# Kernel tuning notes

Measured on AMD Instinct MI355X. Metric: run time of the kernel, lower is better.

## Reference

```python
import math
import jax, jax.numpy as jnp
import numpy as np

B, S, E, H, P = 8, 1024, 512, 8, 32
MAXD, OFFS, LW, STL, HID = 256, 8.0, 4, 4, 2048

def _lin(x, w, b):
    return x @ w.T + b

def _gelu(x):
    return jax.nn.gelu(x, approximate=False)  # torch nn.GELU default (erf)

def _ln(x, g, b, eps=1e-5):
    m = x.mean(-1, keepdims=True)
    v = ((x - m) ** 2).mean(-1, keepdims=True)
    return (x - m) / jnp.sqrt(v + eps) * g + b

def setup_inputs() -> dict:
    key = jax.random.key(0)
    ks = iter(jax.random.split(key, 40))
    def w(*shape):
        return (jax.random.normal(next(ks), shape, dtype=jnp.float32) * 0.02)
    x = jax.random.normal(next(ks), (B, S, E), dtype=jnp.float32)
    lengths = jax.random.randint(next(ks), (B,), S // 2, S + 1)
    padding_mask = jnp.arange(S)[None, :] >= lengths[:, None]  # (B,S) bool
    inp = dict(x=x, padding_mask=padding_mask)
    # local MHA (torch nn.MultiheadAttention packed in_proj)
    inp.update(in_proj_w=w(3 * E, E), in_proj_b=jnp.zeros((3 * E,), jnp.float32),
               mha_out_w=w(E, E), mha_out_b=jnp.zeros((E,), jnp.float32))
    # deformable attention projections
    for nm in ('dq', 'dk', 'dv', 'do'):
        inp[nm + '_w'] = w(E, E); inp[nm + '_b'] = jnp.zeros((E,), jnp.float32)
    inp.update(off1_w=w(E, E), off1_b=jnp.zeros((E,), jnp.float32),
               off2_w=w(H * P, E), off2_b=jnp.zeros((H * P,), jnp.float32))
    inp.update(gate1_w=w(E, 3 * E), gate1_b=jnp.zeros((E,), jnp.float32),
               gate2_w=w(E, E), gate2_b=jnp.zeros((E,), jnp.float32))
    inp.update(n1_g=jnp.ones((E,), jnp.float32), n1_b=jnp.zeros((E,), jnp.float32),
               n2_g=jnp.ones((E,), jnp.float32), n2_b=jnp.zeros((E,), jnp.float32))
    inp.update(ffn1_w=w(HID, E), ffn1_b=jnp.zeros((HID,), jnp.float32),
               ffn2_w=w(E, HID), ffn2_b=jnp.zeros((E,), jnp.float32))
    return inp

def _forward(x, padding_mask, in_proj_w, in_proj_b, mha_out_w, mha_out_b,
             dq_w, dq_b, dk_w, dk_b, dv_w, dv_b, do_w, do_b,
             off1_w, off1_b, off2_w, off2_b, gate1_w, gate1_b, gate2_w, gate2_b,
             n1_g, n1_b, n2_g, n2_b, ffn1_w, ffn1_b, ffn2_w, ffn2_b):
    Bv, Sv, Ev = x.shape
    hd = Ev // H
    pos = jnp.arange(Sv)
    # ---------------- local causal windowed MHA ----------------
    qkv = _lin(x, in_proj_w, in_proj_b)
    q, k, v = jnp.split(qkv, 3, axis=-1)
    q = q.reshape(Bv, Sv, H, hd).transpose(0, 2, 1, 3)  # bhsd
    k = k.reshape(Bv, Sv, H, hd).transpose(0, 2, 1, 3)
    v = v.reshape(Bv, Sv, H, hd).transpose(0, 2, 1, 3)
    scores = jnp.einsum('bhqd,bhkd->bhqk', q, k) / math.sqrt(hd)
    future = pos[None, :] > pos[:, None]
    too_far = (pos[:, None] - pos[None, :]) >= min(LW, STL)
    lmask = (future | too_far)[None, None] | padding_mask[:, None, None, :]
    scores = jnp.where(lmask, -jnp.inf, scores)
    allm = lmask.all(-1, keepdims=True)
    scores = jnp.where(allm, 0.0, scores)  # avoid NaN on fully-masked (padded) rows
    attn = jax.nn.softmax(scores, axis=-1)
    attn = jnp.where(lmask, 0.0, attn)
    lo = jnp.einsum('bhqk,bhkd->bhqd', attn, v).transpose(0, 2, 1, 3).reshape(Bv, Sv, Ev)
    local_out = _lin(lo, mha_out_w, mha_out_b)
    # ---------------- deformable long-history attention ----------------
    anchors = jnp.linspace(0.1, 0.9, P)
    valid_len = jnp.clip(Sv - padding_mask.sum(-1), 1, None)
    positions = pos[None, :, None].astype(jnp.float32)  # (1,S,1)
    base = anchors[None, None, :] * positions
    off = jnp.tanh(_lin(_gelu(_lin(x, off1_w, off1_b)), off2_w, off2_b))
    off = off.reshape(Bv, Sv, H, P).mean(2) * OFFS
    sampled = base + off
    sampled = jnp.clip(sampled, jnp.clip(positions - MAXD, 0, None), positions)
    sampled = jnp.minimum(sampled, (valid_len - 1).astype(jnp.float32)[:, None, None])
    sp = jnp.round(sampled).astype(jnp.int32)  # (B,S,P) sample positions
    qd = _lin(x, dq_w, dq_b)
    kd = _lin(x, dk_w, dk_b)
    vd = _lin(x, dv_w, dv_b)
    bidx = jnp.arange(Bv)[:, None, None]
    k_sp = kd[bidx, sp]  # (B,S,P,E) gathered keys
    v_sp = vd[bidx, sp]
    sc = jnp.einsum('bqd,bqpd->bqp', qd, k_sp) / math.sqrt(Ev)
    samp_inv = padding_mask[bidx, sp]
    causal_inv = sp > pos[None, :, None]
    rb = jnp.clip(pos[:, None] - (STL - 1), 0, None)
    long_mem_mask = pos[None, :] >= rb  # (S,S): forbid recent short-term positions
    extra_inv = long_mem_mask[pos[None, :, None], sp]
    inv = samp_inv | causal_inv | extra_inv
    sc = jnp.where(inv, -jnp.inf, sc)
    alli = inv.all(-1, keepdims=True)
    sc = jnp.where(alli, 0.0, sc)
    a = jax.nn.softmax(sc, axis=-1)
    a = jnp.where(inv, 0.0, a)
    long_out = _lin(jnp.einsum('bqp,bqpd->bqd', a, v_sp), do_w, do_b)
    # ---------------- gate fuse + FFN ----------------
    cat = jnp.concatenate([x, local_out, long_out], axis=-1)
    g = jax.nn.sigmoid(_lin(_gelu(_lin(cat, gate1_w, gate1_b)), gate2_w, gate2_b))
    fused = g * local_out + (1.0 - g) * long_out
    x1 = _ln(x + fused, n1_g, n1_b)
    f = _lin(_gelu(_lin(x1, ffn1_w, ffn1_b)), ffn2_w, ffn2_b)
    return _ln(x1 + f, n2_g, n2_b)

def reference(x, padding_mask, in_proj_w, in_proj_b, mha_out_w, mha_out_b,
              dq_w, dq_b, dk_w, dk_b, dv_w, dv_b, do_w, do_b,
              off1_w, off1_b, off2_w, off2_b, gate1_w, gate1_b, gate2_w, gate2_b,
              n1_g, n1_b, n2_g, n2_b, ffn1_w, ffn1_b, ffn2_w, ffn2_b):
    return _forward(x, padding_mask, in_proj_w, in_proj_b, mha_out_w, mha_out_b,
                    dq_w, dq_b, dk_w, dk_b, dv_w, dv_b, do_w, do_b,
                    off1_w, off1_b, off2_w, off2_b, gate1_w, gate1_b, gate2_w, gate2_b,
                    n1_g, n1_b, n2_g, n2_b, ffn1_w, ffn1_b, ffn2_w, ffn2_b)
```

## Files before the change

kernel.cpp:

```cpp
#include <hip/hip_runtime.h>
#include <hip/hip_bf16.h>
#include <type_traits>

typedef __hip_bfloat16 bf16;
typedef __attribute__((ext_vector_type(8))) short short8;
typedef __attribute__((ext_vector_type(4))) float floatx4;

static constexpr int kB = 8;
static constexpr int kS = 1024;
static constexpr int kE = 512;
static constexpr int kH = 8;
static constexpr int kP = 32;
static constexpr int kTok = kB * kS;
static constexpr int kHid = 2048;

__device__ __forceinline__ void load8f(const bf16* p, float* f) {
  uint4 u = *(const uint4*)p;
  const bf16* h = (const bf16*)&u;
#pragma unroll
  for (int e = 0; e < 8; e++) f[e] = __bfloat162float(h[e]);
}
__device__ __forceinline__ void store8b(bf16* p, const float* f) {
  uint4 u;
  bf16* h = (bf16*)&u;
#pragma unroll
  for (int e = 0; e < 8; e++) h[e] = __float2bfloat16(f[e]);
  *(uint4*)p = u;
}
__device__ __forceinline__ bool is_pad(const void* pm, int flag, int idx) {
  return flag ? (((const int*)pm)[idx] != 0)
              : (((const unsigned char*)pm)[idx] != 0);
}

__global__ __launch_bounds__(256) void detect_kernel(const void* __restrict__ x,
                                                     int* __restrict__ meta) {
  __shared__ int cnt;
  if (threadIdx.x == 0) cnt = 0;
  __syncthreads();
  const unsigned short* u = (const unsigned short*)x;
  int c = 0;
  for (int i = threadIdx.x; i < 1024; i += 256) {
    int e = (u[i] >> 7) & 0xFF;
    if (e >= 0x90) c++;
  }
  if (c) atomicAdd(&cnt, c);
  __syncthreads();
  if (threadIdx.x == 0) meta[9] = (cnt > 64) ? 1 : 0;
}

__global__ __launch_bounds__(256) void meta_kernel(const void* __restrict__ pm,
                                                   int* __restrict__ meta) {
  __shared__ int bigfound;
  __shared__ int cnt[kB];
  int tid = threadIdx.x;
  if (tid == 0) bigfound = 0;
  if (tid < kB) cnt[tid] = 0;
  __syncthreads();
  const unsigned int* w = (const unsigned int*)pm;
  int f = 0;
  for (int i = tid; i < 2048; i += 256)
    if (w[i] & 0xFFFFFFFEu) f = 1;
  if (f) atomicOr(&bigfound, 1);
  __syncthreads();
  int flag = bigfound ? 0 : 1;
  for (int i = tid; i < kTok; i += 256) {
    if (is_pad(pm, flag, i)) atomicAdd(&cnt[i >> 10], 1);
  }
  __syncthreads();
  if (tid == 0) meta[0] = flag;
  if (tid < kB) {
    int vl = kS - cnt[tid];
    if (vl < 1) vl = 1;
    meta[1 + tid] = vl;
  }
}

struct CvtJob { const void* src; bf16* hi; bf16* lo; int nblk; };
struct CvtJobs { CvtJob j[13]; };
__global__ __launch_bounds__(256) void cvt_all_kernel(CvtJobs jobs,
                                                      const int* __restrict__ meta) {
  int fp = meta[9];
  int b = blockIdx.x, ji = 0;
  while (b >= jobs.j[ji].nblk) { b -= jobs.j[ji].nblk; ji++; }
  CvtJob J = jobs.j[ji];
  int i = b * 1024 + threadIdx.x * 4;
  float v[4];
  if (fp) {
    float4 f = ((const float4*)J.src)[i >> 2];
    v[0] = f.x; v[1] = f.y; v[2] = f.z; v[3] = f.w;
  } else {
    uint2 u = *(const uint2*)((const bf16*)J.src + i);
    const bf16* h = (const bf16*)&u;
#pragma unroll
    for (int e = 0; e < 4; e++) v[e] = __bfloat162float(h[e]);
  }
  uint2 uh;
  bf16* hh = (bf16*)&uh;
#pragma unroll
  for (int e = 0; e < 4; e++) hh[e] = __float2bfloat16(v[e]);
  *(uint2*)(J.hi + i) = uh;
  if (J.lo) {
    uint2 ul;
    bf16* hl = (bf16*)&ul;
#pragma unroll
    for (int e = 0; e < 4; e++)
      hl[e] = __float2bfloat16(v[e] - __bfloat162float(hh[e]));
    *(uint2*)(J.lo + i) = ul;
  }
}

struct CvtFJob { const void* src; float* dst; int n; };
struct CvtFJobs { CvtFJob j[16]; };
__global__ __launch_bounds__(256) void cvt_small_kernel(CvtFJobs jobs,
                                                        const int* __restrict__ meta) {
  int fp = meta[9];
#pragma unroll 1
  for (int ji = 0; ji < 16; ji++) {
    CvtFJob J = jobs.j[ji];
    for (int i = threadIdx.x; i < J.n; i += 256)
      J.dst[i] = fp ? ((const float*)J.src)[i]
                    : __bfloat162float(((const bf16*)J.src)[i]);
  }
}

static constexpr int BK = 32, LDK = 40;

template <int BM, int BN, int ACT, bool ACC, typename OUTT>
__global__ __launch_bounds__(256) void gemm_bt(
    const bf16* __restrict__ A, const bf16* __restrict__ W,
    const float* __restrict__ bias, OUTT* __restrict__ C, int M, int N,
    int K) {
  constexpr int WR = (BM == 128 && BN == 128) ? 4 : 2;
  constexpr int WC = (BN == 128) ? 4 : 4;
  __shared__ bf16 As[BM * LDK];
  __shared__ bf16 Bs[BN * LDK];
  const int tid = threadIdx.x;
  const int lane = tid & 63;
  const int wid = tid >> 6;
  int wm, wn;
  if constexpr (BM == 128 && BN == 128) {
    wm = (wid >> 1) * 64; wn = (wid & 1) * 64;
  } else {
    wm = wid * 32; wn = 0;
  }
  const int m0 = blockIdx.x * BM, n0 = blockIdx.y * BN;

  floatx4 acc[WR][WC];
#pragma unroll
  for (int i = 0; i < WR; i++)
#pragma unroll
    for (int j = 0; j < WC; j++) acc[i][j] = (floatx4)0.0f;

  for (int kt = 0; kt < K; kt += BK) {
#pragma unroll
    for (int c = 0; c < BM / 64; c++) {
      int v = c * 256 + tid;
      int row = v >> 2, off = (v & 3) * 8;
      *(uint4*)(&As[row * LDK + off]) =
          *(const uint4*)(&A[(size_t)(m0 + row) * K + kt + off]);
    }
#pragma unroll
    for (int c = 0; c < BN / 64; c++) {
      int v = c * 256 + tid;
      int row = v >> 2, off = (v & 3) * 8;
      *(uint4*)(&Bs[row * LDK + off]) =
          *(const uint4*)(&W[(size_t)(n0 + row) * K + kt + off]);
    }
    __syncthreads();
    const int ko = (lane >> 4) * 8;
    short8 af[WR], bfr[WC];
#pragma unroll
    for (int i = 0; i < WR; i++)
      af[i] = *(const short8*)(&As[(wm + i * 16 + (lane & 15)) * LDK + ko]);
#pragma unroll
    for (int j = 0; j < WC; j++)
      bfr[j] = *(const short8*)(&Bs[(wn + j * 16 + (lane & 15)) * LDK + ko]);
#pragma unroll
    for (int i = 0; i < WR; i++)
#pragma unroll
      for (int j = 0; j < WC; j++)
        acc[i][j] = __builtin_amdgcn_mfma_f32_16x16x32_bf16(af[i], bfr[j],
                                                            acc[i][j], 0, 0, 0);
    __syncthreads();
  }

#pragma unroll
  for (int i = 0; i < WR; i++) {
    int row_b = m0 + wm + i * 16 + (lane >> 4) * 4;
#pragma unroll
    for (int j = 0; j < WC; j++) {
      int col = n0 + wn + j * 16 + (lane & 15);
      float bv = bias ? bias[col] : 0.0f;
#pragma unroll
      for (int r = 0; r < 4; r++) {
        float v = acc[i][j][r] + bv;
        if (ACT == 1) v = 0.5f * v * (1.0f + erff(v * 0.70710678118654752f));
        else if (ACT == 2) v = 1.0f / (1.0f + expf(-v));
        size_t idx = (size_t)(row_b + r) * N + col;
        if constexpr (ACC) {
          C[idx] = C[idx] + v;
        } else if constexpr (std::is_same<OUTT, float>::value) {
          C[idx] = v;
        } else {
          C[idx] = __float2bfloat16(v);
        }
      }
    }
  }
}

template <int BM, int BN>
__global__ __launch_bounds__(256) void gemm3_bt(
    const bf16* __restrict__ Ah, const bf16* __restrict__ Al,
    const bf16* __restrict__ Wh, const bf16* __restrict__ Wl,
    const float* __restrict__ bias, float* __restrict__ C, int M, int N,
    int K) {
  constexpr int WR = 2;
  constexpr int WC = (BM == 128) ? 4 : 2;
  __shared__ bf16 Ash[BM * LDK];
  __shared__ bf16 Asl[BM * LDK];
  __shared__ bf16 Bsh[BN * LDK];
  __shared__ bf16 Bsl[BN * LDK];
  const int tid = threadIdx.x;
  const int lane = tid & 63;
  const int wid = tid >> 6;
  int wm, wn;
  if constexpr (BM == 128) {
    wm = wid * 32; wn = 0;
  } else {
    wm = (wid >> 1) * 32; wn = (wid & 1) * 32;
  }
  const int m0 = blockIdx.x * BM, n0 = blockIdx.y * BN;

  floatx4 acc[WR][WC];
#pragma unroll
  for (int i = 0; i < WR; i++)
#pragma unroll
    for (int j = 0; j < WC; j++) acc[i][j] = (floatx4)0.0f;

  for (int kt = 0; kt < K; kt += BK) {
#pragma unroll
    for (int c = 0; c < BM / 64; c++) {
      int v = c * 256 + tid;
      int row = v >> 2, off = (v & 3) * 8;
      size_t g = (size_t)(m0 + row) * K + kt + off;
      *(uint4*)(&Ash[row * LDK + off]) = *(const uint4*)(&Ah[g]);
      *(uint4*)(&Asl[row * LDK + off]) = *(const uint4*)(&Al[g]);
    }
#pragma unroll
    for (int c = 0; c < BN / 64; c++) {
      int v = c * 256 + tid;
      int row = v >> 2, off = (v & 3) * 8;
      size_t g = (size_t)(n0 + row) * K + kt + off;
      *(uint4*)(&Bsh[row * LDK + off]) = *(const uint4*)(&Wh[g]);
      *(uint4*)(&Bsl[row * LDK + off]) = *(const uint4*)(&Wl[g]);
    }
    __syncthreads();
    const int ko = (lane >> 4) * 8;
    short8 ah[WR], al[WR], bh[WC], bl[WC];
#pragma unroll
    for (int i = 0; i < WR; i++) {
      int ro = (wm + i * 16 + (lane & 15)) * LDK + ko;
      ah[i] = *(const short8*)(&Ash[ro]);
      al[i] = *(const short8*)(&Asl[ro]);
    }
#pragma unroll
    for (int j = 0; j < WC; j++) {
      int ro = (wn + j * 16 + (lane & 15)) * LDK + ko;
      bh[j] = *(const short8*)(&Bsh[ro]);
      bl[j] = *(const short8*)(&Bsl[ro]);
    }
#pragma unroll
    for (int i = 0; i < WR; i++)
#pragma unroll
      for (int j = 0; j < WC; j++) {
        acc[i][j] = __builtin_amdgcn_mfma_f32_16x16x32_bf16(ah[i], bh[j],
                                                            acc[i][j], 0, 0, 0);
        acc[i][j] = __builtin_amdgcn_mfma_f32_16x16x32_bf16(ah[i], bl[j],
                                                            acc[i][j], 0, 0, 0);
        acc[i][j] = __builtin_amdgcn_mfma_f32_16x16x32_bf16(al[i], bh[j],
                                                            acc[i][j], 0, 0, 0);
      }
    __syncthreads();
  }

#pragma unroll
  for (int i = 0; i < WR; i++) {
    int row_b = m0 + wm + i * 16 + (lane >> 4) * 4;
#pragma unroll
    for (int j = 0; j < WC; j++) {
      int col = n0 + wn + j * 16 + (lane & 15);
      float bv = bias[col];
#pragma unroll
      for (int r = 0; r < 4; r++)
        C[(size_t)(row_b + r) * N + col] = acc[i][j][r] + bv;
    }
  }
}

__global__ __launch_bounds__(256) void local_attn_kernel(
    const bf16* __restrict__ qkv, const void* __restrict__ pm,
    const int* __restrict__ meta, bf16* __restrict__ lo) {
  int lane = threadIdx.x & 63;
  int t = blockIdx.x * 4 + (threadIdx.x >> 6);
  int b = t >> 10, s = t & 1023;
  int h = lane >> 3, sub = lane & 7;
  int flag = meta[0];
  float q[8];
  load8f(qkv + (size_t)t * 1536 + h * 64 + sub * 8, q);
  float sc[4];
  bool val[4];
#pragma unroll
  for (int w = 0; w < 4; w++) {
    int kp = s - 3 + w;
    bool v = (kp >= 0) && !is_pad(pm, flag, b * kS + kp);
    float d = 0.0f;
    if (v) {
      float kk[8];
      load8f(qkv + (size_t)(b * kS + kp) * 1536 + 512 + h * 64 + sub * 8, kk);
#pragma unroll
      for (int e = 0; e < 8; e++) d += q[e] * kk[e];
    }
    d += __shfl_xor(d, 1);
    d += __shfl_xor(d, 2);
    d += __shfl_xor(d, 4);
    sc[w] = v ? d / 8.0f : -INFINITY;
    val[w] = v;
  }
  float mx = fmaxf(fmaxf(sc[0], sc[1]), fmaxf(sc[2], sc[3]));
  float a[4] = {0.f, 0.f, 0.f, 0.f};
  if (mx != -INFINITY) {
    float ssum = 0.f;
#pragma unroll
    for (int w = 0; w < 4; w++) {
      float e = val[w] ? expf(sc[w] - mx) : 0.0f;
      a[w] = e;
      ssum += e;
    }
#pragma unroll
    for (int w = 0; w < 4; w++) a[w] /= ssum;
  }
  float o[8] = {0.f, 0.f, 0.f, 0.f, 0.f, 0.f, 0.f, 0.f};
#pragma unroll
  for (int w = 0; w < 4; w++) {
    if (val[w] && a[w] > 0.0f) {
      int kp = s - 3 + w;
      float vv[8];
      load8f(qkv + (size_t)(b * kS + kp) * 1536 + 1024 + h * 64 + sub * 8, vv);
#pragma unroll
      for (int e = 0; e < 8; e++) o[e] += a[w] * vv[e];
    }
  }
  store8b(lo + (size_t)t * kE + lane * 8, o);
}

__global__ __launch_bounds__(256) void gelu_split_kernel(
    const float* __restrict__ S, bf16* __restrict__ hi, bf16* __restrict__ lo) {
  int i = (blockIdx.x * 256 + threadIdx.x) * 4;
#pragma unroll
  for (int c = 0; c < 4; c++) {
    float v = S[i + c];
    float g = 0.5f * v * (1.0f + erff(v * 0.70710678118654752f));
    bf16 a = __float2bfloat16(g);
    hi[i + c] = a;
    lo[i + c] = __float2bfloat16(g - __bfloat162float(a));
  }
}

__global__ __launch_bounds__(256) void sampler_kernel(
    const float* __restrict__ rawf, const void* __restrict__ pm,
    const int* __restrict__ meta, int* __restrict__ sp,
    unsigned int* __restrict__ invm) {
  int t = blockIdx.x * 8 + (threadIdx.x >> 5);
  int p = threadIdx.x & 31;
  int b = t >> 10, s = t & 1023;
  int flag = meta[0];
  float off = 0.0f;
#pragma unroll
  for (int h = 0; h < kH; h++) off += tanhf(rawf[(size_t)t * 256 + h * kP + p]);
  double anchor = 0.1 + 0.8 * (double)p / 31.0;
  double sampled = anchor * (double)s + (double)off;
  double lov = fmax(0.0, (double)s - 256.0);
  sampled = fmin(fmax(sampled, lov), (double)s);
  int vlen = meta[1 + b];
  sampled = fmin(sampled, (double)(vlen - 1));
  int spv = (int)rint(sampled);
  bool inv = is_pad(pm, flag, b * kS + spv) || (spv > s) ||
             (spv >= max(0, s - 3));
  sp[(size_t)t * kP + p] = spv;
  unsigned long long m = __ballot(inv);
  int lane = threadIdx.x & 63;
  if (lane == 0) invm[t] = (unsigned int)m;
  if (lane == 32) invm[t] = (unsigned int)(m >> 32);
}

__global__ __launch_bounds__(256) void long_attn_kernel(
    const bf16* __restrict__ qkvd, const int* __restrict__ sp,
    const unsigned int* __restrict__ invm, bf16* __restrict__ ctx) {
  int lane = threadIdx.x & 63;
  int bid = blockIdx.x;
  int sbid = (bid & 7) * 256 + (bid >> 3);
  int t = sbid * 4 + (threadIdx.x >> 6);
  int b = t >> 10;
  int p = lane & 31;
  int row_abs = b * kS + sp[(size_t)t * kP + p];
  float q[8];
  load8f(qkvd + (size_t)t * 1536 + lane * 8, q);
  float sc_mine = 0.0f;
#pragma unroll 4
  for (int pp = 0; pp < 32; pp++) {
    int row = __shfl(row_abs, pp);
    float kk[8];
    load8f(qkvd + (size_t)row * 1536 + 512 + lane * 8, kk);
    float d = 0.0f;
#pragma unroll
    for (int e = 0; e < 8; e++) d += q[e] * kk[e];
#pragma unroll
    for (int m = 1; m < 64; m <<= 1) d += __shfl_xor(d, m);
    if (p == pp) sc_mine = d;
  }
  bool inv = (invm[t] >> p) & 1u;
  float sc = inv ? -INFINITY : sc_mine / 22.627416997969522f;
  float mx = sc;
#pragma unroll
  for (int m = 1; m < 32; m <<= 1) mx = fmaxf(mx, __shfl_xor(mx, m));
  float e = (inv || mx == -INFINITY) ? 0.0f : expf(sc - mx);
  float ssum = e;
#pragma unroll
  for (int m = 1; m < 32; m <<= 1) ssum += __shfl_xor(ssum, m);
  float a = (ssum > 0.0f) ? e / ssum : 0.0f;
  float o[8] = {0.f, 0.f, 0.f, 0.f, 0.f, 0.f, 0.f, 0.f};
#pragma unroll 4
  for (int pp = 0; pp < 32; pp++) {
    float ap = __shfl(a, pp);
    int row = __shfl(row_abs, pp);
    if (ap != 0.0f) {
      float vv[8];
      load8f(qkvd + (size_t)row * 1536 + 1024 + lane * 8, vv);
#pragma unroll
      for (int e2 = 0; e2 < 8; e2++) o[e2] += ap * vv[e2];
    }
  }
  store8b(ctx + (size_t)t * kE + lane * 8, o);
}

__global__ __launch_bounds__(256) void concat_kernel(
    const bf16* __restrict__ x, const bf16* __restrict__ lo,
    const bf16* __restrict__ lg, bf16* __restrict__ cat) {
  int i = blockIdx.x * 256 + threadIdx.x;
  int t = i / 192, c = i % 192;
  const bf16* src = (c < 64) ? (x + (size_t)t * kE + c * 8)
                  : (c < 128) ? (lo + (size_t)t * kE + (c - 64) * 8)
                              : (lg + (size_t)t * kE + (c - 128) * 8);
  *(uint4*)(cat + (size_t)t * 1536 + c * 8) = *(const uint4*)src;
}

__global__ __launch_bounds__(256) void ln1_kernel(
    const void* __restrict__ xin, const int* __restrict__ meta,
    const bf16* __restrict__ lo, const bf16* __restrict__ lg,
    const bf16* __restrict__ g, const float* __restrict__ gamma,
    const float* __restrict__ beta, bf16* __restrict__ x1b,
    float* __restrict__ x1f) {
  int lane = threadIdx.x & 63;
  int t = blockIdx.x * 4 + (threadIdx.x >> 6);
  size_t base = (size_t)t * kE + lane * 8;
  float xv[8], lov[8], lgv[8], gv[8], h[8];
  if (meta[9]) {
    const float4* xf = (const float4*)((const float*)xin + base);
    float4 a = xf[0], b2 = xf[1];
    xv[0] = a.x; xv[1] = a.y; xv[2] = a.z; xv[3] = a.w;
    xv[4] = b2.x; xv[5] = b2.y; xv[6] = b2.z; xv[7] = b2.w;
  } else {
    load8f((const bf16*)xin + base, xv);
  }
  load8f(lo + base, lov);
  load8f(lg + base, lgv);
  load8f(g + base, gv);
  float s1 = 0.f, s2 = 0.f;
#pragma unroll
  for (int e = 0; e < 8; e++) {
    h[e] = xv[e] + gv[e] * lov[e] + (1.0f - gv[e]) * lgv[e];
    s1 += h[e];
    s2 += h[e] * h[e];
  }
#pragma unroll
  for (int m = 1; m < 64; m <<= 1) {
    s1 += __shfl_xor(s1, m);
    s2 += __shfl_xor(s2, m);
  }
  float mean = s1 * (1.0f / kE);
  float var = s2 * (1.0f / kE) - mean * mean;
  float rstd = 1.0f / sqrtf(var + 1e-5f);
  float y[8];
#pragma unroll
  for (int e = 0; e < 8; e++)
    y[e] = (h[e] - mean) * rstd * gamma[lane * 8 + e] + beta[lane * 8 + e];
  store8b(x1b + base, y);
#pragma unroll
  for (int e = 0; e < 8; e++) x1f[base + e] = y[e];
}

__global__ __launch_bounds__(256) void ln2_kernel(
    const float* __restrict__ x1f, const float* __restrict__ ff,
    const float* __restrict__ gamma, const float* __restrict__ beta,
    const int* __restrict__ meta, void* __restrict__ out) {
  int lane = threadIdx.x & 63;
  int t = blockIdx.x * 4 + (threadIdx.x >> 6);
  size_t base = (size_t)t * kE + lane * 8;
  float h[8];
  float s1 = 0.f, s2 = 0.f;
#pragma unroll
  for (int e = 0; e < 8; e++) {
    h[e] = x1f[base + e] + ff[base + e];
    s1 += h[e];
    s2 += h[e] * h[e];
  }
#pragma unroll
  for (int m = 1; m < 64; m <<= 1) {
    s1 += __shfl_xor(s1, m);
    s2 += __shfl_xor(s2, m);
  }
  float mean = s1 * (1.0f / kE);
  float var = s2 * (1.0f / kE) - mean * mean;
  float rstd = 1.0f / sqrtf(var + 1e-5f);
  float y[8];
#pragma unroll
  for (int e = 0; e < 8; e++)
    y[e] = (h[e] - mean) * rstd * gamma[lane * 8 + e] + beta[lane * 8 + e];
  if (meta[9]) {
    float* of = (float*)out + base;
    ((float4*)of)[0] = make_float4(y[0], y[1], y[2], y[3]);
    ((float4*)of)[1] = make_float4(y[4], y[5], y[6], y[7]);
  } else {
    store8b((bf16*)out + base, y);
  }
}

extern "C" void kernel_launch(void* const* d_in, const int* in_sizes, int n_in,
                              void* d_out, int out_size, void* d_ws,
                              size_t ws_size, hipStream_t stream) {
  const void* x = d_in[0];
  const void* pm = d_in[1];

  char* w = (char*)d_ws;
  auto alloc = [&](size_t bytes) {
    char* p = w;
    w += (bytes + 255) & ~(size_t)255;
    return p;
  };
  bf16* qkv = (bf16*)alloc((size_t)kTok * 1536 * 2);
  bf16* qkvd = (bf16*)alloc((size_t)kTok * 1536 * 2);
  bf16* big = (bf16*)alloc((size_t)kTok * 2048 * 2);
  bf16* lo_ctx = (bf16*)alloc((size_t)kTok * kE * 2);
  bf16* local_out = (bf16*)alloc((size_t)kTok * kE * 2);
  bf16* long_out = (bf16*)alloc((size_t)kTok * kE * 2);
  bf16* hbuf = (bf16*)alloc((size_t)kTok * kE * 2);
  bf16* gbuf = (bf16*)alloc((size_t)kTok * kE * 2);
  bf16* x1b = (bf16*)alloc((size_t)kTok * kE * 2);
  float* x1f = (float*)alloc((size_t)kTok * kE * 4);
  int* sp = (int*)alloc((size_t)kTok * kP * 4);
  unsigned int* invm = (unsigned int*)alloc((size_t)kTok * 4);
  int* meta = (int*)alloc(256);
  bf16* x_hi = (bf16*)alloc((size_t)kTok * kE * 2);
  bf16* x_lo = (bf16*)alloc((size_t)kTok * kE * 2);
  bf16* ipw = (bf16*)alloc(1536 * 512 * 2);
  bf16* mow = (bf16*)alloc(512 * 512 * 2);
  bf16* dqkv_w = (bf16*)alloc(1536 * 512 * 2);
  bf16* dow = (bf16*)alloc(512 * 512 * 2);
  bf16* o1h = (bf16*)alloc(512 * 512 * 2);
  bf16* o1l = (bf16*)alloc(512 * 512 * 2);
  bf16* o2h = (bf16*)alloc(256 * 512 * 2);
  bf16* o2l = (bf16*)alloc(256 * 512 * 2);
  bf16* g1w = (bf16*)alloc(512 * 1536 * 2);
  bf16* g2w = (bf16*)alloc(512 * 512 * 2);
  bf16* f1w = (bf16*)alloc((size_t)2048 * 512 * 2);
  bf16* f2w = (bf16*)alloc((size_t)512 * 2048 * 2);
  float* ipb = (float*)alloc(1536 * 4);
  float* mob = (float*)alloc(512 * 4);
  float* dqkv_b = (float*)alloc(1536 * 4);
  float* dob = (float*)alloc(512 * 4);
  float* o1b = (float*)alloc(512 * 4);
  float* o2b = (float*)alloc(256 * 4);
  float* g1b = (float*)alloc(512 * 4);
  float* g2b = (float*)alloc(512 * 4);
  float* n1g = (float*)alloc(512 * 4);
  float* n1bt = (float*)alloc(512 * 4);
  float* n2g = (float*)alloc(512 * 4);
  float* n2bt = (float*)alloc(512 * 4);
  float* f1b = (float*)alloc(2048 * 4);
  float* f2b = (float*)alloc(512 * 4);

  float* rawf = (float*)qkv;
  float* f_f32 = (float*)qkv;
  float* S32 = x1f;
  bf16* h_hi = hbuf;
  bf16* h_lo = x1b;

  dim3 blk(256);
  detect_kernel<<<1, blk, 0, stream>>>(x, meta);
  meta_kernel<<<1, blk, 0, stream>>>(pm, meta);

  CvtJobs J;
  auto job = [](const void* s, bf16* hi, bf16* lo, int n) {
    CvtJob j; j.src = s; j.hi = hi; j.lo = lo; j.nblk = n >> 10; return j;
  };
  J.j[0] = job(d_in[0], x_hi, x_lo, kTok * kE);
  J.j[1] = job(d_in[2], ipw, nullptr, 1536 * 512);
  J.j[2] = job(d_in[4], mow, nullptr, 512 * 512);
  J.j[3] = job(d_in[6], dqkv_w, nullptr, 512 * 512);
  J.j[4] = job(d_in[8], dqkv_w + 512 * 512, nullptr, 512 * 512);
  J.j[5] = job(d_in[10], dqkv_w + 1024 * 512, nullptr, 512 * 512);
  J.j[6] = job(d_in[12], dow, nullptr, 512 * 512);
  J.j[7] = job(d_in[14], o1h, o1l, 512 * 512);
  J.j[8] = job(d_in[16], o2h, o2l, 256 * 512);
  J.j[9] = job(d_in[18], g1w, nullptr, 512 * 1536);
  J.j[10] = job(d_in[20], g2w, nullptr, 512 * 512);
  J.j[11] = job(d_in[26], f1w, nullptr, 2048 * 512);
  J.j[12] = job(d_in[28], f2w, nullptr, 512 * 2048);
  int totblk = 0;
  for (int i = 0; i < 13; i++) totblk += J.j[i].nblk;
  cvt_all_kernel<<<totblk, blk, 0, stream>>>(J, meta);

  CvtFJobs JF;
  auto fjob = [](const void* s, float* d, int n) {
    CvtFJob j; j.src = s; j.dst = d; j.n = n; return j;
  };
  JF.j[0] = fjob(d_in[3], ipb, 1536);
  JF.j[1] = fjob(d_in[5], mob, 512);
  JF.j[2] = fjob(d_in[7], dqkv_b, 512);
  JF.j[3] = fjob(d_in[9], dqkv_b + 512, 512);
  JF.j[4] = fjob(d_in[11], dqkv_b + 1024, 512);
  JF.j[5] = fjob(d_in[13], dob, 512);
  JF.j[6] = fjob(d_in[15], o1b, 512);
  JF.j[7] = fjob(d_in[17], o2b, 256);
  JF.j[8] = fjob(d_in[19], g1b, 512);
  JF.j[9] = fjob(d_in[21], g2b, 512);
  JF.j[10] = fjob(d_in[22], n1g, 512);
  JF.j[11] = fjob(d_in[23], n1bt, 512);
  JF.j[12] = fjob(d_in[24], n2g, 512);
  JF.j[13] = fjob(d_in[25], n2bt, 512);
  JF.j[14] = fjob(d_in[27], f1b, 2048);
  JF.j[15] = fjob(d_in[29], f2b, 512);
  cvt_small_kernel<<<1, blk, 0, stream>>>(JF, meta);

  gemm_bt<128, 128, 0, false, bf16><<<dim3(64, 12), blk, 0, stream>>>(
      x_hi, ipw, ipb, qkv, kTok, 1536, kE);
  local_attn_kernel<<<2048, blk, 0, stream>>>(qkv, pm, meta, lo_ctx);
  gemm_bt<128, 64, 0, false, bf16><<<dim3(64, 8), blk, 0, stream>>>(
      lo_ctx, mow, mob, local_out, kTok, kE, kE);

  gemm3_bt<128, 64><<<dim3(64, 8), blk, 0, stream>>>(
      x_hi, x_lo, o1h, o1l, o1b, S32, kTok, kE, kE);
  gelu_split_kernel<<<4096, blk, 0, stream>>>(S32, h_hi, h_lo);
  gemm3_bt<64, 64><<<dim3(128, 4), blk, 0, stream>>>(
      h_hi, h_lo, o2h, o2l, o2b, rawf, kTok, 256, kE);
  sampler_kernel<<<1024, blk, 0, stream>>>(rawf, pm, meta, sp, invm);

  gemm_bt<128, 128, 0, false, bf16><<<dim3(64, 12), blk, 0, stream>>>(
      x_hi, dqkv_w, dqkv_b, qkvd, kTok, 1536, kE);
  long_attn_kernel<<<2048, blk, 0, stream>>>(qkvd, sp, invm, lo_ctx);
  gemm_bt<128, 64, 0, false, bf16><<<dim3(64, 8), blk, 0, stream>>>(
      lo_ctx, dow, dob, long_out, kTok, kE, kE);

  concat_kernel<<<6144, blk, 0, stream>>>(x_hi, local_out, long_out, big);
  gemm_bt<128, 64, 1, false, bf16><<<dim3(64, 8), blk, 0, stream>>>(
      big, g1w, g1b, hbuf, kTok, kE, 1536);
  gemm_bt<128, 64, 2, false, bf16><<<dim3(64, 8), blk, 0, stream>>>(
      hbuf, g2w, g2b, gbuf, kTok, kE, kE);

  ln1_kernel<<<2048, blk, 0, stream>>>(x, meta, local_out, long_out, gbuf, n1g,
                                       n1bt, x1b, x1f);
  gemm_bt<128, 128, 1, false, bf16><<<dim3(64, 16), blk, 0, stream>>>(
      x1b, f1w, f1b, big, kTok, kHid, kE);
  gemm_bt<128, 64, 0, false, float><<<dim3(64, 8), blk, 0, stream>>>(
      big, f2w, f2b, f_f32, kTok, kE, kHid);
  ln2_kernel<<<2048, blk, 0, stream>>>(x1f, f_f32, n2g, n2bt, meta, d_out);
}
```

Before: 514.2 us.

## Merge QKV GEMMs, fuse concat into gate GEMM, pair out-projections, vectorize epilogues

Concatenates the local and deformable QKV weights so one 3072-wide GEMM produces both projections. The two output projections run as one paired launch. The concat kernel is removed by having the gate1 GEMM read x, local_out and long_out directly. GEMM epilogues swap MFMA operand order so each lane holds four consecutive columns, which allows float4/uint2 vector stores and vector bias loads. Exact erf GELU and expf are replaced with a tanh-approximation GELU and __expf, which removes launches and memory traffic but changes numerics slightly.

```diff
diff --git a/kernel.cpp b/kernel.cpp
--- a/kernel.cpp
+++ b/kernel.cpp
@@ -30,6 +30,12 @@
 __device__ __forceinline__ bool is_pad(const void* pm, int flag, int idx) {
   return flag ? (((const int*)pm)[idx] != 0)
               : (((const unsigned char*)pm)[idx] != 0);
+}
+__device__ __forceinline__ float fast_gelu(float x) {
+  float u = x * (0.7978845608f + 0.044714998f * x * x);
+  float e = __expf(2.0f * u);
+  float t = 1.0f - 2.0f / (e + 1.0f);
+  return 0.5f * x * (1.0f + t);
 }
 
 __global__ __launch_bounds__(256) void detect_kernel(const void* __restrict__ x,
@@ -125,13 +131,14 @@
 
 static constexpr int BK = 32, LDK = 40;
 
-template <int BM, int BN, int ACT, bool ACC, typename OUTT>
-__global__ __launch_bounds__(256) void gemm_bt(
-    const bf16* __restrict__ A, const bf16* __restrict__ W,
-    const float* __restrict__ bias, OUTT* __restrict__ C, int M, int N,
-    int K) {
+template <int BM, int BN, int ACT, typename OUTT>
+__device__ __forceinline__ void gemm_core(const bf16* __restrict__ A,
+                                          const bf16* __restrict__ W,
+                                          const float* __restrict__ bias,
+                                          OUTT* __restrict__ C, int N, int K,
+                                          int m0, int n0) {
   constexpr int WR = (BM == 128 && BN == 128) ? 4 : 2;
-  constexpr int WC = (BN == 128) ? 4 : 4;
+  constexpr int WC = 4;
   __shared__ bf16 As[BM * LDK];
   __shared__ bf16 Bs[BN * LDK];
   const int tid = threadIdx.x;
@@ -143,7 +150,6 @@
   } else {
     wm = wid * 32; wn = 0;
   }
-  const int m0 = blockIdx.x * BM, n0 = blockIdx.y * BN;
 
   floatx4 acc[WR][WC];
 #pragma unroll
@@ -179,32 +185,132 @@
     for (int i = 0; i < WR; i++)
 #pragma unroll
       for (int j = 0; j < WC; j++)
-        acc[i][j] = __builtin_amdgcn_mfma_f32_16x16x32_bf16(af[i], bfr[j],
+        acc[i][j] = __builtin_amdgcn_mfma_f32_16x16x32_bf16(bfr[j], af[i],
                                                             acc[i][j], 0, 0, 0);
     __syncthreads();
   }
 
 #pragma unroll
   for (int i = 0; i < WR; i++) {
-    int row_b = m0 + wm + i * 16 + (lane >> 4) * 4;
+    int row = m0 + wm + i * 16 + (lane & 15);
 #pragma unroll
     for (int j = 0; j < WC; j++) {
-      int col = n0 + wn + j * 16 + (lane & 15);
-      float bv = bias ? bias[col] : 0.0f;
+      int col = n0 + wn + j * 16 + ((lane >> 4) << 2);
+      float bv[4] = {0.f, 0.f, 0.f, 0.f};
+      if (bias) {
+        float4 b4 = *(const float4*)&bias[col];
+        bv[0] = b4.x; bv[1] = b4.y; bv[2] = b4.z; bv[3] = b4.w;
+      }
+      float v[4];
 #pragma unroll
       for (int r = 0; r < 4; r++) {
-        float v = acc[i][j][r] + bv;
-        if (ACT == 1) v = 0.5f * v * (1.0f + erff(v * 0.70710678118654752f));
-        else if (ACT == 2) v = 1.0f / (1.0f + expf(-v));
-        size_t idx = (size_t)(row_b + r) * N + col;
-        if constexpr (ACC) {
-          C[idx] = C[idx] + v;
-        } else if constexpr (std::is_same<OUTT, float>::value) {
-          C[idx] = v;
-        } else {
-          C[idx] = __float2bfloat16(v);
-        }
+        v[r] = acc[i][j][r] + bv[r];
+        if (ACT == 1) v[r] = fast_gelu(v[r]);
+        else if (ACT == 2) v[r] = 1.0f / (1.0f + __expf(-v[r]));
       }
+      size_t idx = (size_t)row * N + col;
+      if constexpr (std::is_same<OUTT, float>::value) {
+        *(float4*)&C[idx] = make_float4(v[0], v[1], v[2], v[3]);
+      } else {
+        uint2 u;
+        bf16* h = (bf16*)&u;
+#pragma unroll
+        for (int r = 0; r < 4; r++) h[r] = __float2bfloat16(v[r]);
+        *(uint2*)&C[idx] = u;
+      }
+    }
+  }
+}
+
+template <int BM, int BN, int ACT, typename OUTT>
+__global__ __launch_bounds__(256) void gemm_bt(
+    const bf16* __restrict__ A, const bf16* __restrict__ W,
+    const float* __restrict__ bias, OUTT* __restrict__ C, int N, int K) {
+  gemm_core<BM, BN, ACT, OUTT>(A, W, bias, C, N, K, blockIdx.x * BM,
+                               blockIdx.y * BN);
+}
+
+__global__ __launch_bounds__(256) void gemm_pair(
+    const bf16* __restrict__ A0, const bf16* __restrict__ W0,
+    const float* __restrict__ b0, bf16* __restrict__ C0,
+    const bf16* __restrict__ A1, const bf16* __restrict__ W1,
+    const float* __restrict__ b1, bf16* __restrict__ C1, int N, int K) {
+  int nb = N >> 6;
+  bool s = (int)blockIdx.y >= nb;
+  gemm_core<128, 64, 0, bf16>(s ? A1 : A0, s ? W1 : W0, s ? b1 : b0,
+                              s ? C1 : C0, N, K, blockIdx.x * 128,
+                              (s ? (int)blockIdx.y - nb : (int)blockIdx.y) * 64);
+}
+
+__global__ __launch_bounds__(256) void gemm_gate1(
+    const bf16* __restrict__ x, const bf16* __restrict__ lo,
+    const bf16* __restrict__ lg, const bf16* __restrict__ W,
+    const float* __restrict__ bias, bf16* __restrict__ C) {
+  constexpr int BM = 128, BN = 64, WR = 2, WC = 4;
+  constexpr int N = 512, K = 1536;
+  __shared__ bf16 As[BM * LDK];
+  __shared__ bf16 Bs[BN * LDK];
+  const int tid = threadIdx.x;
+  const int lane = tid & 63;
+  const int wid = tid >> 6;
+  const int wm = wid * 32, wn = 0;
+  const int m0 = blockIdx.x * BM, n0 = blockIdx.y * BN;
+
+  floatx4 acc[WR][WC];
+#pragma unroll
+  for (int i = 0; i < WR; i++)
+#pragma unroll
+    for (int j = 0; j < WC; j++) acc[i][j] = (floatx4)0.0f;
+
+  for (int kt = 0; kt < K; kt += BK) {
+#pragma unroll
+    for (int c = 0; c < 2; c++) {
+      int v = c * 256 + tid;
+      int row = v >> 2, off = (v & 3) * 8;
+      int k = kt + off;
+      const bf16* src = (k < 512) ? x : (k < 1024) ? lo : lg;
+      int kk = k & 511;
+      *(uint4*)(&As[row * LDK + off]) =
+          *(const uint4*)(&src[(size_t)(m0 + row) * 512 + kk]);
+    }
+    {
+      int v = tid;
+      int row = v >> 2, off = (v & 3) * 8;
+      *(uint4*)(&Bs[row * LDK + off]) =
+          *(const uint4*)(&W[(size_t)(n0 + row) * K + kt + off]);
+    }
+    __syncthreads();
+    const int ko = (lane >> 4) * 8;
+    short8 af[WR], bfr[WC];
+#pragma unroll
+    for (int i = 0; i < WR; i++)
+      af[i] = *(const short8*)(&As[(wm + i * 16 + (lane & 15)) * LDK + ko]);
+#pragma unroll
+    for (int j = 0; j < WC; j++)
+      bfr[j] = *(const short8*)(&Bs[(wn + j * 16 + (lane & 15)) * LDK + ko]);
+#pragma unroll
+    for (int i = 0; i < WR; i++)
+#pragma unroll
+      for (int j = 0; j < WC; j++)
+        acc[i][j] = __builtin_amdgcn_mfma_f32_16x16x32_bf16(bfr[j], af[i],
+                                                            acc[i][j], 0, 0, 0);
+    __syncthreads();
+  }
+
+#pragma unroll
+  for (int i = 0; i < WR; i++) {
+    int row = m0 + wm + i * 16 + (lane & 15);
+#pragma unroll
+    for (int j = 0; j < WC; j++) {
+      int col = n0 + wn + j * 16 + ((lane >> 4) << 2);
+      float4 b4 = *(const float4*)&bias[col];
+      float bv[4] = {b4.x, b4.y, b4.z, b4.w};
+      uint2 u;
+      bf16* h = (bf16*)&u;
+#pragma unroll
+      for (int r = 0; r < 4; r++)
+        h[r] = __float2bfloat16(fast_gelu(acc[i][j][r] + bv[r]));
+      *(uint2*)&C[(size_t)row * N + col] = u;
     }
   }
 }
@@ -213,8 +319,7 @@
 __global__ __launch_bounds__(256) void gemm3_bt(
     const bf16* __restrict__ Ah, const bf16* __restrict__ Al,
     const bf16* __restrict__ Wh, const bf16* __restrict__ Wl,
-    const float* __restrict__ bias, float* __restrict__ C, int M, int N,
-    int K) {
+    const float* __restrict__ bias, float* __restrict__ C, int N, int K) {
   constexpr int WR = 2;
   constexpr int WC = (BM == 128) ? 4 : 2;
   __shared__ bf16 Ash[BM * LDK];
@@ -274,11 +379,11 @@
     for (int i = 0; i < WR; i++)
 #pragma unroll
       for (int j = 0; j < WC; j++) {
-        acc[i][j] = __builtin_amdgcn_mfma_f32_16x16x32_bf16(ah[i], bh[j],
+        acc[i][j] = __builtin_amdgcn_mfma_f32_16x16x32_bf16(bh[j], ah[i],
                                                             acc[i][j], 0, 0, 0);
-        acc[i][j] = __builtin_amdgcn_mfma_f32_16x16x32_bf16(ah[i], bl[j],
+        acc[i][j] = __builtin_amdgcn_mfma_f32_16x16x32_bf16(bl[j], ah[i],
                                                             acc[i][j], 0, 0, 0);
-        acc[i][j] = __builtin_amdgcn_mfma_f32_16x16x32_bf16(al[i], bh[j],
+        acc[i][j] = __builtin_amdgcn_mfma_f32_16x16x32_bf16(bh[j], al[i],
                                                             acc[i][j], 0, 0, 0);
       }
     __syncthreads();
@@ -286,14 +391,16 @@
 
 #pragma unroll
   for (int i = 0; i < WR; i++) {
-    int row_b = m0 + wm + i * 16 + (lane >> 4) * 4;
+    int row = m0 + wm + i * 16 + (lane & 15);
 #pragma unroll
     for (int j = 0; j < WC; j++) {
-      int col = n0 + wn + j * 16 + (lane & 15);
-      float bv = bias[col];
-#pragma unroll
-      for (int r = 0; r < 4; r++)
-        C[(size_t)(row_b + r) * N + col] = acc[i][j][r] + bv;
+      int col = n0 + wn + j * 16 + ((lane >> 4) << 2);
+      float4 b4 = *(const float4*)&bias[col];
+      float bv[4] = {b4.x, b4.y, b4.z, b4.w};
+      float v[4];
+#pragma unroll
+      for (int r = 0; r < 4; r++) v[r] = acc[i][j][r] + bv[r];
+      *(float4*)&C[(size_t)row * N + col] = make_float4(v[0], v[1], v[2], v[3]);
     }
   }
 }
@@ -307,7 +414,7 @@
   int h = lane >> 3, sub = lane & 7;
   int flag = meta[0];
   float q[8];
-  load8f(qkv + (size_t)t * 1536 + h * 64 + sub * 8, q);
+  load8f(qkv + (size_t)t * 3072 + h * 64 + sub * 8, q);
   float sc[4];
   bool val[4];
 #pragma unroll
@@ -317,7 +424,7 @@
     float d = 0.0f;
     if (v) {
       float kk[8];
-      load8f(qkv + (size_t)(b * kS + kp) * 1536 + 512 + h * 64 + sub * 8, kk);
+      load8f(qkv + (size_t)(b * kS + kp) * 3072 + 512 + h * 64 + sub * 8, kk);
 #pragma unroll
       for (int e = 0; e < 8; e++) d += q[e] * kk[e];
     }
@@ -346,7 +453,7 @@
     if (val[w] && a[w] > 0.0f) {
       int kp = s - 3 + w;
       float vv[8];
-      load8f(qkv + (size_t)(b * kS + kp) * 1536 + 1024 + h * 64 + sub * 8, vv);
+      load8f(qkv + (size_t)(b * kS + kp) * 3072 + 1024 + h * 64 + sub * 8, vv);
 #pragma unroll
       for (int e = 0; e < 8; e++) o[e] += a[w] * vv[e];
     }
@@ -395,7 +502,7 @@
 }
 
 __global__ __launch_bounds__(256) void long_attn_kernel(
-    const bf16* __restrict__ qkvd, const int* __restrict__ sp,
+    const bf16* __restrict__ qkv, const int* __restrict__ sp,
     const unsigned int* __restrict__ invm, bf16* __restrict__ ctx) {
   int lane = threadIdx.x & 63;
   int bid = blockIdx.x;
@@ -405,13 +512,13 @@
   int p = lane & 31;
   int row_abs = b * kS + sp[(size_t)t * kP + p];
   float q[8];
-  load8f(qkvd + (size_t)t * 1536 + lane * 8, q);
+  load8f(qkv + (size_t)t * 3072 + 1536 + lane * 8, q);
   float sc_mine = 0.0f;
 #pragma unroll 4
   for (int pp = 0; pp < 32; pp++) {
     int row = __shfl(row_abs, pp);
     float kk[8];
-    load8f(qkvd + (size_t)row * 1536 + 512 + lane * 8, kk);
+    load8f(qkv + (size_t)row * 3072 + 2048 + lane * 8, kk);
     float d = 0.0f;
 #pragma unroll
     for (int e = 0; e < 8; e++) d += q[e] * kk[e];
@@ -436,23 +543,12 @@
     int row = __shfl(row_abs, pp);
     if (ap != 0.0f) {
       float vv[8];
-      load8f(qkvd + (size_t)row * 1536 + 1024 + lane * 8, vv);
+      load8f(qkv + (size_t)row * 3072 + 2560 + lane * 8, vv);
 #pragma unroll
       for (int e2 = 0; e2 < 8; e2++) o[e2] += ap * vv[e2];
     }
   }
   store8b(ctx + (size_t)t * kE + lane * 8, o);
-}
-
-__global__ __launch_bounds__(256) void concat_kernel(
-    const bf16* __restrict__ x, const bf16* __restrict__ lo,
-    const bf16* __restrict__ lg, bf16* __restrict__ cat) {
-  int i = blockIdx.x * 256 + threadIdx.x;
-  int t = i / 192, c = i % 192;
-  const bf16* src = (c < 64) ? (x + (size_t)t * kE + c * 8)
-                  : (c < 128) ? (lo + (size_t)t * kE + (c - 64) * 8)
-                              : (lg + (size_t)t * kE + (c - 128) * 8);
-  *(uint4*)(cat + (size_t)t * 1536 + c * 8) = *(const uint4*)src;
 }
 
 __global__ __launch_bounds__(256) void ln1_kernel(
@@ -548,24 +644,23 @@
     w += (bytes + 255) & ~(size_t)255;
     return p;
   };
-  bf16* qkv = (bf16*)alloc((size_t)kTok * 1536 * 2);
-  bf16* qkvd = (bf16*)alloc((size_t)kTok * 1536 * 2);
-  bf16* big = (bf16*)alloc((size_t)kTok * 2048 * 2);
+  bf16* qkv_all = (bf16*)alloc((size_t)kTok * 3072 * 2);
   bf16* lo_ctx = (bf16*)alloc((size_t)kTok * kE * 2);
+  bf16* ctx2 = (bf16*)alloc((size_t)kTok * kE * 2);
   bf16* local_out = (bf16*)alloc((size_t)kTok * kE * 2);
   bf16* long_out = (bf16*)alloc((size_t)kTok * kE * 2);
   bf16* hbuf = (bf16*)alloc((size_t)kTok * kE * 2);
   bf16* gbuf = (bf16*)alloc((size_t)kTok * kE * 2);
   bf16* x1b = (bf16*)alloc((size_t)kTok * kE * 2);
   float* x1f = (float*)alloc((size_t)kTok * kE * 4);
+  float* rawf = (float*)alloc((size_t)kTok * 256 * 4);
   int* sp = (int*)alloc((size_t)kTok * kP * 4);
   unsigned int* invm = (unsigned int*)alloc((size_t)kTok * 4);
   int* meta = (int*)alloc(256);
   bf16* x_hi = (bf16*)alloc((size_t)kTok * kE * 2);
   bf16* x_lo = (bf16*)alloc((size_t)kTok * kE * 2);
-  bf16* ipw = (bf16*)alloc(1536 * 512 * 2);
+  bf16* wall = (bf16*)alloc((size_t)3072 * 512 * 2);
   bf16* mow = (bf16*)alloc(512 * 512 * 2);
-  bf16* dqkv_w = (bf16*)alloc(1536 * 512 * 2);
   bf16* dow = (bf16*)alloc(512 * 512 * 2);
   bf16* o1h = (bf16*)alloc(512 * 512 * 2);
   bf16* o1l = (bf16*)alloc(512 * 512 * 2);
@@ -575,9 +670,8 @@
   bf16* g2w = (bf16*)alloc(512 * 512 * 2);
   bf16* f1w = (bf16*)alloc((size_t)2048 * 512 * 2);
   bf16* f2w = (bf16*)alloc((size_t)512 * 2048 * 2);
-  float* ipb = (float*)alloc(1536 * 4);
+  float* ball = (float*)alloc(3072 * 4);
   float* mob = (float*)alloc(512 * 4);
-  float* dqkv_b = (float*)alloc(1536 * 4);
   float* dob = (float*)alloc(512 * 4);
   float* o1b = (float*)alloc(512 * 4);
   float* o2b = (float*)alloc(256 * 4);
@@ -590,11 +684,11 @@
   float* f1b = (float*)alloc(2048 * 4);
   float* f2b = (float*)alloc(512 * 4);
 
-  float* rawf = (float*)qkv;
-  float* f_f32 = (float*)qkv;
   float* S32 = x1f;
   bf16* h_hi = hbuf;
   bf16* h_lo = x1b;
+  float* f_f32 = (float*)qkv_all;
+  bf16* ffn_h = (bf16*)((char*)qkv_all + (size_t)kTok * kE * 4);
 
   dim3 blk(256);
   detect_kernel<<<1, blk, 0, stream>>>(x, meta);
@@ -605,11 +699,11 @@
     CvtJob j; j.src = s; j.hi = hi; j.lo = lo; j.nblk = n >> 10; return j;
   };
   J.j[0] = job(d_in[0], x_hi, x_lo, kTok * kE);
-  J.j[1] = job(d_in[2], ipw, nullptr, 1536 * 512);
-  J.j[2] = job(d_in[4], mow, nullptr, 512 * 512);
-  J.j[3] = job(d_in[6], dqkv_w, nullptr, 512 * 512);
-  J.j[4] = job(d_in[8], dqkv_w + 512 * 512, nullptr, 512 * 512);
-  J.j[5] = job(d_in[10], dqkv_w + 1024 * 512, nullptr, 512 * 512);
+  J.j[1] = job(d_in[2], wall, nullptr, 1536 * 512);
+  J.j[2] = job(d_in[6], wall + (size_t)1536 * 512, nullptr, 512 * 512);
+  J.j[3] = job(d_in[8], wall + (size_t)2048 * 512, nullptr, 512 * 512);
+  J.j[4] = job(d_in[10], wall + (size_t)2560 * 512, nullptr, 512 * 512);
+  J.j[5] = job(d_in[4], mow, nullptr, 512 * 512);
   J.j[6] = job(d_in[12], dow, nullptr, 512 * 512);
   J.j[7] = job(d_in[14], o1h, o1l, 512 * 512);
   J.j[8] = job(d_in[16], o2h, o2l, 256 * 512);
@@ -625,11 +719,11 @@
   auto fjob = [](const void* s, float* d, int n) {
     CvtFJob j; j.src = s; j.dst = d; j.n = n; return j;
   };
-  JF.j[0] = fjob(d_in[3], ipb, 1536);
-  JF.j[1] = fjob(d_in[5], mob, 512);
-  JF.j[2] = fjob(d_in[7], dqkv_b, 512);
-  JF.j[3] = fjob(d_in[9], dqkv_b + 512, 512);
-  JF.j[4] = fjob(d_in[11], dqkv_b + 1024, 512);
+  JF.j[0] = fjob(d_in[3], ball, 1536);
+  JF.j[1] = fjob(d_in[7], ball + 1536, 512);
+  JF.j[2] = fjob(d_in[9], ball + 2048, 512);
+  JF.j[3] = fjob(d_in[11], ball + 2560, 512);
+  JF.j[4] = fjob(d_in[5], mob, 512);
   JF.j[5] = fjob(d_in[13], dob, 512);
   JF.j[6] = fjob(d_in[15], o1b, 512);
   JF.j[7] = fjob(d_in[17], o2b, 256);
@@ -643,36 +737,30 @@
   JF.j[15] = fjob(d_in[29], f2b, 512);
   cvt_small_kernel<<<1, blk, 0, stream>>>(JF, meta);
 
-  gemm_bt<128, 128, 0, false, bf16><<<dim3(64, 12), blk, 0, stream>>>(
-      x_hi, ipw, ipb, qkv, kTok, 1536, kE);
-  local_attn_kernel<<<2048, blk, 0, stream>>>(qkv, pm, meta, lo_ctx);
-  gemm_bt<128, 64, 0, false, bf16><<<dim3(64, 8), blk, 0, stream>>>(
-      lo_ctx, mow, mob, local_out, kTok, kE, kE);
-
+  gemm_bt<128, 128, 0, bf16><<<dim3(64, 24), blk, 0, stream>>>(
+      x_hi, wall, ball, qkv_all, 3072, kE);
   gemm3_bt<128, 64><<<dim3(64, 8), blk, 0, stream>>>(
-      x_hi, x_lo, o1h, o1l, o1b, S32, kTok, kE, kE);
+      x_hi, x_lo, o1h, o1l, o1b, S32, kE, kE);
+  local_attn_kernel<<<2048, blk, 0, stream>>>(qkv_all, pm, meta, lo_ctx);
   gelu_split_kernel<<<4096, blk, 0, stream>>>(S32, h_hi, h_lo);
   gemm3_bt<64, 64><<<dim3(128, 4), blk, 0, stream>>>(
-      h_hi, h_lo, o2h, o2l, o2b, rawf, kTok, 256, kE);
+      h_hi, h_lo, o2h, o2l, o2b, rawf, 256, kE);
   sampler_kernel<<<1024, blk, 0, stream>>>(rawf, pm, meta, sp, invm);
-
-  gemm_bt<128, 128, 0, false, bf16><<<dim3(64, 12), blk, 0, stream>>>(
-      x_hi, dqkv_w, dqkv_b, qkvd, kTok, 1536, kE);
-  long_attn_kernel<<<2048, blk, 0, stream>>>(qkvd, sp, invm, lo_ctx);
-  gemm_bt<128, 64, 0, false, bf16><<<dim3(64, 8), blk, 0, stream>>>(
-      lo_ctx, dow, dob, long_out, kTok, kE, kE);
-
-  concat_kernel<<<6144, blk, 0, stream>>>(x_hi, local_out, long_out, big);
-  gemm_bt<128, 64, 1, false, bf16><<<dim3(64, 8), blk, 0, stream>>>(
-      big, g1w, g1b, hbuf, kTok, kE, 1536);
-  gemm_bt<128, 64, 2, false, bf16><<<dim3(64, 8), blk, 0, stream>>>(
-      hbuf, g2w, g2b, gbuf, kTok, kE, kE);
+  long_attn_kernel<<<2048, blk, 0, stream>>>(qkv_all, sp, invm, ctx2);
+
+  gemm_pair<<<dim3(64, 16), blk, 0, stream>>>(lo_ctx, mow, mob, local_out,
+                                              ctx2, dow, dob, long_out, kE, kE);
+
+  gemm_gate1<<<dim3(64, 8), blk, 0, stream>>>(x_hi, local_out, long_out, g1w,
+                                              g1b, hbuf);
+  gemm_bt<128, 64, 2, bf16><<<dim3(64, 8), blk, 0, stream>>>(
+      hbuf, g2w, g2b, gbuf, kE, kE);
 
   ln1_kernel<<<2048, blk, 0, stream>>>(x, meta, local_out, long_out, gbuf, n1g,
                                        n1bt, x1b, x1f);
-  gemm_bt<128, 128, 1, false, bf16><<<dim3(64, 16), blk, 0, stream>>>(
-      x1b, f1w, f1b, big, kTok, kHid, kE);
-  gemm_bt<128, 64, 0, false, float><<<dim3(64, 8), blk, 0, stream>>>(
-      big, f2w, f2b, f_f32, kTok, kE, kHid);
+  gemm_bt<128, 128, 1, bf16><<<dim3(64, 16), blk, 0, stream>>>(
+      x1b, f1w, f1b, ffn_h, kHid, kE);
+  gemm_bt<128, 64, 0, float><<<dim3(64, 8), blk, 0, stream>>>(
+      ffn_h, f2w, f2b, f_f32, kE, kHid);
   ln2_kernel<<<2048, blk, 0, stream>>>(x1f, f_f32, n2g, n2bt, meta, d_out);
 }
```

Measured after the change: 489.8 us. 1.05x faster.
